# Optimization experiments

Hardware: AMD Instinct MI355X
Metric: run time of the kernel (lower is better)

## Reference

```python
import jax, jax.numpy as jnp
import numpy as np

N = 100000
E = 1600000
D_IN = 128
D_OUT = 128


def setup_inputs() -> dict:
    key = jax.random.key(0)
    k1, k2, k3, k4, k5, k6 = jax.random.split(key, 6)
    h = jax.random.normal(k1, (N, D_IN), dtype=jnp.float32)
    # deg^{-1/2}-style positive per-node normalization, shape [N,1]
    norm = jax.random.uniform(k2, (N, 1), dtype=jnp.float32, minval=0.05, maxval=1.0)
    weight = jax.random.normal(k3, (D_IN, D_OUT), dtype=jnp.float32) * (1.0 / np.sqrt(D_IN))
    bias = jax.random.normal(k4, (D_OUT,), dtype=jnp.float32) * 0.01
    src = jax.random.randint(k5, (E,), 0, N, dtype=jnp.int32)
    dst = jax.random.randint(k6, (E,), 0, N, dtype=jnp.int32)
    return {"h": h, "norm": norm, "weight": weight, "bias": bias, "src": src, "dst": dst}


def reference(h, norm, weight, bias, src, dst):
    # m = (h @ W) * norm   (per-source-node message)
    m = jnp.matmul(h, weight) * norm            # [N, D_OUT]
    # copy_src + sum: scatter-sum messages from src nodes into dst nodes
    n = jax.ops.segment_sum(m[src], dst, num_segments=h.shape[0])  # [N, D_OUT]
    # destination-side normalization, bias, LeakyReLU(0.2)
    n = n * norm + bias
    return jax.nn.leaky_relu(n, negative_slope=0.2)
```

## Files before the change

### kernel.cpp

```cpp
#include <hip/hip_runtime.h>

#define N_NODES 100000
#define E_EDGES 1600000
#define D 128
#define SHIFT 7
#define BNODES 128
#define NB ((N_NODES + BNODES - 1) / BNODES)

#define CNT_CHUNK 2048
#define CNT_NBLK ((E_EDGES + CNT_CHUNK - 1) / CNT_CHUNK)
#define PREP_NBLK (N_NODES * 32 / 256)
#define SCAT_CHUNK 8192
#define SCAT_PASS 2
#define SCAT_NBLK ((E_EDGES + SCAT_CHUNK - 1) / SCAT_CHUNK)
#define GATH32_NBLK (N_NODES / 8)

#define FBLK 64
#define FGRID ((N_NODES + FBLK - 1) / FBLK)

#define GROWS 64
#define KCH 32

typedef _Float16       f16x8  __attribute__((ext_vector_type(8)));
typedef float          f32x4  __attribute__((ext_vector_type(4)));
typedef unsigned short u16x8  __attribute__((ext_vector_type(8)));

#define WS_CNT   0
#define WS_BOFF  784
#define WS_POS   1568
#define WS_NOFF  2352
#define WS_EBUF  102400
#define WS_ESRC  (102400 + E_EDGES)
#define WS_HS    (102400 + 2 * E_EDGES)
#define WS_FULL_INTS ((size_t)WS_HS + (size_t)N_NODES * D / 2)
#define WS_MID_INTS  ((size_t)WS_HS)

__global__ __launch_bounds__(256) void prep_count(const float* __restrict__ h,
                                                  const float* __restrict__ norm,
                                                  unsigned short* __restrict__ hs,
                                                  const int* __restrict__ dst,
                                                  int* __restrict__ cnt,
                                                  int prep_blocks) {
    __shared__ int hist[NB];
    const int t = threadIdx.x;
    if ((int)blockIdx.x < prep_blocks) {
        const int idx = blockIdx.x * 256 + t;
        const int node = idx >> 5;
        const int c = (idx & 31) << 2;
        const float nv = norm[node];
        const float4 v = *reinterpret_cast<const float4*>(h + node * D + c);
        float a[4] = {v.x * nv, v.y * nv, v.z * nv, v.w * nv};
        ushort4 o;
        unsigned short* op = reinterpret_cast<unsigned short*>(&o);
        #pragma unroll
        for (int i = 0; i < 4; ++i) {
            unsigned int u = __float_as_uint(a[i]);
            u += 0x7FFFu + ((u >> 16) & 1u);
            op[i] = (unsigned short)(u >> 16);
        }
        *reinterpret_cast<ushort4*>(hs + node * D + c) = o;
        return;
    }
    const int cb = blockIdx.x - prep_blocks;
    const int e0 = cb * CNT_CHUNK;
    const int rem = (E_EDGES - e0 < CNT_CHUNK) ? (E_EDGES - e0) : CNT_CHUNK;
    for (int i = t; i < NB; i += 256) hist[i] = 0;
    __syncthreads();
    if (rem == CNT_CHUNK) {
        const int4* d4 = reinterpret_cast<const int4*>(dst + e0);
        #pragma unroll
        for (int p = 0; p < 2; ++p) {
            const int4 v = d4[p * 256 + t];
            atomicAdd(&hist[v.x >> SHIFT], 1);
            atomicAdd(&hist[v.y >> SHIFT], 1);
            atomicAdd(&hist[v.z >> SHIFT], 1);
            atomicAdd(&hist[v.w >> SHIFT], 1);
        }
    } else {
        for (int i = t; i < rem; i += 256)
            atomicAdd(&hist[dst[e0 + i] >> SHIFT], 1);
    }
    __syncthreads();
    for (int b = t; b < NB; b += 256) {
        const int c = hist[b];
        if (c) atomicAdd(&cnt[b], c);
    }
}

__global__ __launch_bounds__(1024) void coarse_scan(const int* __restrict__ cnt,
                                                    int* __restrict__ boff,
                                                    int* __restrict__ pos) {
    __shared__ int buf[2][1024];
    const int t = threadIdx.x;
    const int v = (t < NB) ? cnt[t] : 0;
    int pi = 0;
    buf[0][t] = v;
    __syncthreads();
    #pragma unroll
    for (int o = 1; o < 1024; o <<= 1) {
        const int nv = buf[pi][t] + (t >= o ? buf[pi][t - o] : 0);
        buf[1 - pi][t] = nv;
        pi = 1 - pi;
        __syncthreads();
    }
    if (t < NB) {
        const int excl = buf[pi][t] - v;
        boff[t] = excl;
        pos[t] = excl;
    }
    if (t == 0) boff[NB] = E_EDGES;
}

__global__ __launch_bounds__(1024) void coarse_scatter(const int* __restrict__ src,
                                                       const int* __restrict__ dst,
                                                       int* __restrict__ pos,
                                                       int* __restrict__ ebuf) {
    __shared__ int hist[NB];
    const int t = threadIdx.x;
    const int e0 = blockIdx.x * SCAT_CHUNK;
    const int rem = (E_EDGES - e0 < SCAT_CHUNK) ? (E_EDGES - e0) : SCAT_CHUNK;
    for (int i = t; i < NB; i += 1024) hist[i] = 0;
    __syncthreads();
    if (rem == SCAT_CHUNK) {
        const int4* d4 = reinterpret_cast<const int4*>(dst + e0);
        #pragma unroll
        for (int p = 0; p < SCAT_PASS; ++p) {
            const int4 v = d4[p * 1024 + t];
            atomicAdd(&hist[v.x >> SHIFT], 1);
            atomicAdd(&hist[v.y >> SHIFT], 1);
            atomicAdd(&hist[v.z >> SHIFT], 1);
            atomicAdd(&hist[v.w >> SHIFT], 1);
        }
    } else {
        for (int i = t; i < rem; i += 1024)
            atomicAdd(&hist[dst[e0 + i] >> SHIFT], 1);
    }
    __syncthreads();
    for (int b = t; b < NB; b += 1024) {
        const int c = hist[b];
        if (c) hist[b] = atomicAdd(&pos[b], c);
    }
    __syncthreads();
    if (rem == SCAT_CHUNK) {
        const int4* d4 = reinterpret_cast<const int4*>(dst + e0);
        const int4* s4 = reinterpret_cast<const int4*>(src + e0);
        #pragma unroll
        for (int p = 0; p < SCAT_PASS; ++p) {
            const int4 dv = d4[p * 1024 + t];
            const int4 sv = s4[p * 1024 + t];
            int pz;
            pz = atomicAdd(&hist[dv.x >> SHIFT], 1);
            ebuf[pz] = (sv.x << SHIFT) | (dv.x & (BNODES - 1));
            pz = atomicAdd(&hist[dv.y >> SHIFT], 1);
            ebuf[pz] = (sv.y << SHIFT) | (dv.y & (BNODES - 1));
            pz = atomicAdd(&hist[dv.z >> SHIFT], 1);
            ebuf[pz] = (sv.z << SHIFT) | (dv.z & (BNODES - 1));
            pz = atomicAdd(&hist[dv.w >> SHIFT], 1);
            ebuf[pz] = (sv.w << SHIFT) | (dv.w & (BNODES - 1));
        }
    } else {
        for (int i = t; i < rem; i += 1024) {
            const int d = dst[e0 + i];
            const int b = d >> SHIFT;
            const int p = atomicAdd(&hist[b], 1);
            ebuf[p] = (src[e0 + i] << SHIFT) | (d & (BNODES - 1));
        }
    }
}

__global__ __launch_bounds__(256) void bin_sort(const int* __restrict__ boff,
                                                const int* __restrict__ ebuf,
                                                int* __restrict__ esrc,
                                                int* __restrict__ noff) {
    __shared__ int hist[BNODES];
    __shared__ int curs[BNODES];
    __shared__ int sbuf[2][BNODES];
    const int t = threadIdx.x;
    const int bin = blockIdx.x;
    if (t < BNODES) hist[t] = 0;
    __syncthreads();
    const int b0 = boff[bin];
    const int b1 = boff[bin + 1];
    for (int i = b0 + t; i < b1; i += 256)
        atomicAdd(&hist[ebuf[i] & (BNODES - 1)], 1);
    __syncthreads();
    if (t < BNODES) sbuf[0][t] = hist[t];
    __syncthreads();
    int pi = 0;
    #pragma unroll
    for (int o = 1; o < BNODES; o <<= 1) {
        if (t < BNODES)
            sbuf[1 - pi][t] = sbuf[pi][t] + (t >= o ? sbuf[pi][t - o] : 0);
        pi = 1 - pi;
        __syncthreads();
    }
    if (t < BNODES) {
        const int base = b0 + sbuf[pi][t] - hist[t];
        curs[t] = base;
        const int node = (bin << SHIFT) + t;
        if (node < N_NODES) noff[node] = base;
    }
    if (bin == 0 && t == 0) noff[N_NODES] = E_EDGES;
    __syncthreads();
    for (int i = b0 + t; i < b1; i += 256) {
        const int w = ebuf[i];
        const int p = atomicAdd(&curs[w & (BNODES - 1)], 1);
        esrc[p] = w >> SHIFT;
    }
}

__device__ __forceinline__ void wprep_body(int tid, const float* __restrict__ Wm,
                                           f16x8* __restrict__ Whs) {
    const int kiter = tid >> 9;
    const int nt = (tid >> 6) & 7;
    const int lane = tid & 63;
    const int q = lane >> 4;
    const int col = nt * 16 + (lane & 15);
    f16x8 v;
    #pragma unroll
    for (int j = 0; j < 8; ++j)
        v[j] = (_Float16)Wm[(kiter * 32 + q * 8 + j) * D + col];
    Whs[tid] = v;
}

__global__ __launch_bounds__(256) void fused_gather_gemm(
    const unsigned short* __restrict__ hs, const int* __restrict__ noff,
    const int* __restrict__ esrc, const float* __restrict__ Wm,
    const float* __restrict__ bias, const float* __restrict__ norm,
    float* __restrict__ out)
{
    __shared__ _Float16 gs[FBLK][136];
    __shared__ f16x8 Wlds[2048];
    const int t = threadIdx.x;
    const int row0 = blockIdx.x * FBLK;
    const int c = (t & 15) << 3;

    #pragma unroll 1
    for (int r = 0; r < 4; ++r) {
        const int nl = r * 16 + (t >> 4);
        const int node = row0 + nl;
        float a[8];
        #pragma unroll
        for (int j = 0; j < 8; ++j) a[j] = 0.f;
        if (node < N_NODES) {
            int i = noff[node];
            const int end = noff[node + 1];
            for (; i + 7 < end; i += 8) {
                const int s0 = esrc[i];     const int s1 = esrc[i + 1];
                const int s2 = esrc[i + 2]; const int s3 = esrc[i + 3];
                const int s4 = esrc[i + 4]; const int s5 = esrc[i + 5];
                const int s6 = esrc[i + 6]; const int s7 = esrc[i + 7];
                const u16x8 u0 = *reinterpret_cast<const u16x8*>(hs + s0 * D + c);
                const u16x8 u1 = *reinterpret_cast<const u16x8*>(hs + s1 * D + c);
                const u16x8 u2 = *reinterpret_cast<const u16x8*>(hs + s2 * D + c);
                const u16x8 u3 = *reinterpret_cast<const u16x8*>(hs + s3 * D + c);
                const u16x8 u4 = *reinterpret_cast<const u16x8*>(hs + s4 * D + c);
                const u16x8 u5 = *reinterpret_cast<const u16x8*>(hs + s5 * D + c);
                const u16x8 u6 = *reinterpret_cast<const u16x8*>(hs + s6 * D + c);
                const u16x8 u7 = *reinterpret_cast<const u16x8*>(hs + s7 * D + c);
                #pragma unroll
                for (int j = 0; j < 8; ++j) {
                    a[j] += __uint_as_float((unsigned int)u0[j] << 16);
                    a[j] += __uint_as_float((unsigned int)u1[j] << 16);
                    a[j] += __uint_as_float((unsigned int)u2[j] << 16);
                    a[j] += __uint_as_float((unsigned int)u3[j] << 16);
                    a[j] += __uint_as_float((unsigned int)u4[j] << 16);
                    a[j] += __uint_as_float((unsigned int)u5[j] << 16);
                    a[j] += __uint_as_float((unsigned int)u6[j] << 16);
                    a[j] += __uint_as_float((unsigned int)u7[j] << 16);
                }
            }
            if (i + 3 < end) {
                const int s0 = esrc[i];     const int s1 = esrc[i + 1];
                const int s2 = esrc[i + 2]; const int s3 = esrc[i + 3];
                const u16x8 u0 = *reinterpret_cast<const u16x8*>(hs + s0 * D + c);
                const u16x8 u1 = *reinterpret_cast<const u16x8*>(hs + s1 * D + c);
                const u16x8 u2 = *reinterpret_cast<const u16x8*>(hs + s2 * D + c);
                const u16x8 u3 = *reinterpret_cast<const u16x8*>(hs + s3 * D + c);
                #pragma unroll
                for (int j = 0; j < 8; ++j) {
                    a[j] += __uint_as_float((unsigned int)u0[j] << 16);
                    a[j] += __uint_as_float((unsigned int)u1[j] << 16);
                    a[j] += __uint_as_float((unsigned int)u2[j] << 16);
                    a[j] += __uint_as_float((unsigned int)u3[j] << 16);
                }
                i += 4;
            }
            for (; i < end; ++i) {
                const int s = esrc[i];
                const u16x8 u = *reinterpret_cast<const u16x8*>(hs + s * D + c);
                #pragma unroll
                for (int j = 0; j < 8; ++j)
                    a[j] += __uint_as_float((unsigned int)u[j] << 16);
            }
        }
        f16x8 o;
        #pragma unroll
        for (int j = 0; j < 8; ++j) o[j] = (_Float16)a[j];
        *reinterpret_cast<f16x8*>(&gs[nl][c]) = o;
    }

    #pragma unroll 1
    for (int e = t; e < 2048; e += 256) {
        const int kiter = e >> 9;
        const int nt = (e >> 6) & 7;
        const int lane = e & 63;
        const int q = lane >> 4;
        const int col = nt * 16 + (lane & 15);
        f16x8 v;
        #pragma unroll
        for (int j = 0; j < 8; ++j)
            v[j] = (_Float16)Wm[(kiter * 32 + q * 8 + j) * D + col];
        Wlds[e] = v;
    }
    __syncthreads();

    const int lane = t & 63;
    const int strip = t >> 6;
    const int q = lane >> 4;
    const int l15 = lane & 15;

    f32x4 acc[8];
    #pragma unroll
    for (int i = 0; i < 8; ++i) acc[i] = (f32x4){0.f, 0.f, 0.f, 0.f};

    #pragma unroll
    for (int kiter = 0; kiter < 4; ++kiter) {
        const f16x8 a =
            *reinterpret_cast<const f16x8*>(&gs[strip * 16 + l15][kiter * 32 + q * 8]);
        #pragma unroll
        for (int nt = 0; nt < 8; ++nt) {
            const f16x8 b = Wlds[(kiter * 8 + nt) * 64 + lane];
            acc[nt] = __builtin_amdgcn_mfma_f32_16x16x32_f16(a, b, acc[nt], 0, 0, 0);
        }
    }

    float nrm[4];
    int mr[4];
    #pragma unroll
    for (int rgi = 0; rgi < 4; ++rgi) {
        mr[rgi] = row0 + strip * 16 + q * 4 + rgi;
        nrm[rgi] = (mr[rgi] < N_NODES) ? norm[mr[rgi]] : 0.f;
    }
    #pragma unroll
    for (int nt = 0; nt < 8; ++nt) {
        const int col = nt * 16 + l15;
        const float bc = bias[col];
        #pragma unroll
        for (int rgi = 0; rgi < 4; ++rgi) {
            if (mr[rgi] < N_NODES) {
                float v = acc[nt][rgi] * nrm[rgi] + bc;
                v = v > 0.f ? v : 0.2f * v;
                out[mr[rgi] * D + col] = v;
            }
        }
    }
}

__global__ __launch_bounds__(256) void gather_fp32(const float* __restrict__ h,
                                                   const float* __restrict__ norm,
                                                   const int* __restrict__ noff,
                                                   const int* __restrict__ esrc,
                                                   float* __restrict__ g,
                                                   const float* __restrict__ Wm,
                                                   f16x8* __restrict__ Whs) {
    if ((int)blockIdx.x >= GATH32_NBLK) {
        wprep_body((blockIdx.x - GATH32_NBLK) * 256 + threadIdx.x, Wm, Whs);
        return;
    }
    const int t = threadIdx.x;
    const int node = blockIdx.x * 8 + (t >> 5);
    const int c = (t & 31) << 2;
    const int beg = noff[node];
    const int end = noff[node + 1];
    float4 acc = make_float4(0.f, 0.f, 0.f, 0.f);
    for (int i = beg; i < end; ++i) {
        const int s = esrc[i];
        const float nv = norm[s];
        const float4 hv = *reinterpret_cast<const float4*>(h + s * D + c);
        acc.x += hv.x * nv;
        acc.y += hv.y * nv;
        acc.z += hv.z * nv;
        acc.w += hv.w * nv;
    }
    *reinterpret_cast<float4*>(g + node * D + c) = acc;
}

__global__ __launch_bounds__(256) void scatter_kernel(
    const float* __restrict__ h, const float* __restrict__ norm,
    const int* __restrict__ src, const int* __restrict__ dst,
    float* __restrict__ g)
{
    const int idx = blockIdx.x * 256 + threadIdx.x;
    const int e = idx >> 5;
    const int c = (idx & 31) << 2;
    const int s = src[e];
    const int d = dst[e];
    const float nv = norm[s];
    const float4 hv = *reinterpret_cast<const float4*>(h + s * D + c);
    float* gp = g + d * D + c;
    atomicAdd(gp + 0, hv.x * nv);
    atomicAdd(gp + 1, hv.y * nv);
    atomicAdd(gp + 2, hv.z * nv);
    atomicAdd(gp + 3, hv.w * nv);
}

__global__ __launch_bounds__(256) void gemm_mfma(
    float* __restrict__ out, const f16x8* __restrict__ Whs,
    const float* __restrict__ bias, const float* __restrict__ norm)
{
    __shared__ f16x8 Wlds[2048];
    const int t = threadIdx.x;
    const int row0 = blockIdx.x * 64;

    #pragma unroll
    for (int p = 0; p < 8; ++p)
        reinterpret_cast<float4*>(Wlds)[p * 256 + t] =
            reinterpret_cast<const float4*>(Whs)[p * 256 + t];
    __syncthreads();

    const int lane = t & 63;
    const int strip = t >> 6;
    const int q = lane >> 4;
    const int l15 = lane & 15;

    int mrow = row0 + strip * 16 + l15;
    if (mrow >= N_NODES) mrow = N_NODES - 1;

    f32x4 acc[8];
    #pragma unroll
    for (int i = 0; i < 8; ++i) acc[i] = (f32x4){0.f, 0.f, 0.f, 0.f};

    #pragma unroll
    for (int kiter = 0; kiter < 4; ++kiter) {
        const float* gp = out + mrow * D + kiter * 32 + q * 8;
        const float4 ga = *reinterpret_cast<const float4*>(gp);
        const float4 gb = *reinterpret_cast<const float4*>(gp + 4);
        f16x8 a;
        a[0] = (_Float16)ga.x; a[1] = (_Float16)ga.y;
        a[2] = (_Float16)ga.z; a[3] = (_Float16)ga.w;
        a[4] = (_Float16)gb.x; a[5] = (_Float16)gb.y;
        a[6] = (_Float16)gb.z; a[7] = (_Float16)gb.w;
        #pragma unroll
        for (int nt = 0; nt < 8; ++nt) {
            const f16x8 b = Wlds[(kiter * 8 + nt) * 64 + lane];
            acc[nt] = __builtin_amdgcn_mfma_f32_16x16x32_f16(a, b, acc[nt], 0, 0, 0);
        }
    }

    float nrm[4];
    int mr[4];
    #pragma unroll
    for (int rgi = 0; rgi < 4; ++rgi) {
        mr[rgi] = row0 + strip * 16 + q * 4 + rgi;
        nrm[rgi] = (mr[rgi] < N_NODES) ? norm[mr[rgi]] : 0.f;
    }
    #pragma unroll
    for (int nt = 0; nt < 8; ++nt) {
        const int col = nt * 16 + l15;
        const float bc = bias[col];
        #pragma unroll
        for (int rgi = 0; rgi < 4; ++rgi) {
            if (mr[rgi] < N_NODES) {
                float v = acc[nt][rgi] * nrm[rgi] + bc;
                v = v > 0.f ? v : 0.2f * v;
                out[mr[rgi] * D + col] = v;
            }
        }
    }
}

__global__ __launch_bounds__(256) void gemm_epilogue(
    float* __restrict__ out, const float* __restrict__ Wm,
    const float* __restrict__ bias, const float* __restrict__ norm)
{
    __shared__ float gs[GROWS][D + 4];
    __shared__ float Wlds[KCH][D];
    const int t = threadIdx.x;
    const int row0 = blockIdx.x * GROWS;

    #pragma unroll
    for (int p = 0; p < 8; ++p) {
        const int i = p * 256 + t;
        const int r = i >> 5;
        const int c = (i & 31) << 2;
        int gr = row0 + r;
        if (gr >= N_NODES) gr = N_NODES - 1;
        const float4 v = *reinterpret_cast<const float4*>(out + gr * D + c);
        *reinterpret_cast<float4*>(&gs[r][c]) = v;
    }

    const int rg = (t >> 5) * 8;
    const int cb = (t & 31) << 2;

    float4 acc[8];
    #pragma unroll
    for (int i = 0; i < 8; ++i) acc[i] = make_float4(0.f, 0.f, 0.f, 0.f);

    for (int kc = 0; kc < D; kc += KCH) {
        __syncthreads();
        #pragma unroll
        for (int p = 0; p < 4; ++p) {
            const int i = p * 256 + t;
            const int kk = i >> 5;
            const int c = (i & 31) << 2;
            *reinterpret_cast<float4*>(&Wlds[kk][c]) =
                *reinterpret_cast<const float4*>(Wm + (kc + kk) * D + c);
        }
        __syncthreads();

        #pragma unroll
        for (int k4 = 0; k4 < KCH; k4 += 4) {
            float4 wv[4];
            #pragma unroll
            for (int kk = 0; kk < 4; ++kk)
                wv[kk] = *reinterpret_cast<const float4*>(&Wlds[k4 + kk][cb]);
            #pragma unroll
            for (int i = 0; i < 8; ++i) {
                const float4 gv = *reinterpret_cast<const float4*>(&gs[rg + i][kc + k4]);
                acc[i].x += gv.x * wv[0].x; acc[i].y += gv.x * wv[0].y;
                acc[i].z += gv.x * wv[0].z; acc[i].w += gv.x * wv[0].w;
                acc[i].x += gv.y * wv[1].x; acc[i].y += gv.y * wv[1].y;
                acc[i].z += gv.y * wv[1].z; acc[i].w += gv.y * wv[1].w;
                acc[i].x += gv.z * wv[2].x; acc[i].y += gv.z * wv[2].y;
                acc[i].z += gv.z * wv[2].z; acc[i].w += gv.z * wv[2].w;
                acc[i].x += gv.w * wv[3].x; acc[i].y += gv.w * wv[3].y;
                acc[i].z += gv.w * wv[3].z; acc[i].w += gv.w * wv[3].w;
            }
        }
    }

    const float4 b = *reinterpret_cast<const float4*>(bias + cb);
    #pragma unroll
    for (int i = 0; i < 8; ++i) {
        const int gr = row0 + rg + i;
        if (gr < N_NODES) {
            const float nv = norm[gr];
            float4 v;
            v.x = acc[i].x * nv + b.x;
            v.y = acc[i].y * nv + b.y;
            v.z = acc[i].z * nv + b.z;
            v.w = acc[i].w * nv + b.w;
            v.x = v.x > 0.f ? v.x : 0.2f * v.x;
            v.y = v.y > 0.f ? v.y : 0.2f * v.y;
            v.z = v.z > 0.f ? v.z : 0.2f * v.z;
            v.w = v.w > 0.f ? v.w : 0.2f * v.w;
            *reinterpret_cast<float4*>(out + gr * D + cb) = v;
        }
    }
}

extern "C" void kernel_launch(void* const* d_in, const int* in_sizes, int n_in,
                              void* d_out, int out_size, void* d_ws, size_t ws_size,
                              hipStream_t stream) {
    const float* h    = (const float*)d_in[0];
    const float* norm = (const float*)d_in[1];
    const float* Wm   = (const float*)d_in[2];
    const float* bias = (const float*)d_in[3];
    const int*   src  = (const int*)d_in[4];
    const int*   dst  = (const int*)d_in[5];
    float* out = (float*)d_out;
    int* ws = (int*)d_ws;

    if (ws_size >= WS_MID_INTS * 4) {
        int* cnt  = ws + WS_CNT;
        int* boff = ws + WS_BOFF;
        int* pos  = ws + WS_POS;
        int* noff = ws + WS_NOFF;
        int* ebuf = ws + WS_EBUF;
        int* esrc = ws + WS_ESRC;
        unsigned short* hs = (unsigned short*)(ws + WS_HS);
        f16x8* Whs = (f16x8*)ebuf;
        const bool use_bf16 = (ws_size >= WS_FULL_INTS * 4);

        hipMemsetAsync(cnt, 0, NB * sizeof(int), stream);
        if (use_bf16) {
            prep_count<<<PREP_NBLK + CNT_NBLK, 256, 0, stream>>>(h, norm, hs, dst, cnt, PREP_NBLK);
        } else {
            prep_count<<<CNT_NBLK, 256, 0, stream>>>(h, norm, hs, dst, cnt, 0);
        }
        coarse_scan   <<<1, 1024, 0, stream>>>(cnt, boff, pos);
        coarse_scatter<<<SCAT_NBLK, 1024, 0, stream>>>(src, dst, pos, ebuf);
        bin_sort      <<<NB, 256, 0, stream>>>(boff, ebuf, esrc, noff);
        if (use_bf16) {
            fused_gather_gemm<<<FGRID, 256, 0, stream>>>(hs, noff, esrc, Wm, bias, norm, out);
        } else {
            gather_fp32<<<GATH32_NBLK + 8, 256, 0, stream>>>(h, norm, noff, esrc, out, Wm, Whs);
            gemm_mfma<<<(N_NODES + 63) / 64, 256, 0, stream>>>(out, Whs, bias, norm);
        }
    } else {
        hipMemsetAsync(out, 0, (size_t)N_NODES * D * sizeof(float), stream);
        scatter_kernel<<<(E_EDGES * 32) / 256, 256, 0, stream>>>(h, norm, src, dst, out);
        gemm_epilogue<<<(N_NODES + GROWS - 1) / GROWS, 256, 0, stream>>>(out, Wm, bias, norm);
    }
}
```

Baseline: 255.6 us.

## Fuse preprocessing and sorting stages into one cooperative kernel with grid syncs

Replaces the memset, count, scan, coarse scatter and bin sort launches with a single cooperative kernel of 1024 blocks that separates the phases with grid-wide syncs. This removes several launch gaps and intermediate kernel boundaries. The scatter phase now recomputes its per-chunk histogram instead of reusing the one from counting. Separately, the gather-GEMM kernel stages W into LDS in two halves so its shared-memory footprint shrinks, which may raise occupancy at the cost of an extra sync. If the cooperative launch fails, the code falls back to the original multi-kernel path.

```diff
diff --git a/kernel.cpp b/kernel.cpp
--- a/kernel.cpp
+++ b/kernel.cpp
@@ -1,4 +1,7 @@
 #include <hip/hip_runtime.h>
+#include <hip/hip_cooperative_groups.h>
+
+namespace cg = cooperative_groups;
 
 #define N_NODES 100000
 #define E_EDGES 1600000
@@ -14,6 +17,10 @@
 #define SCAT_PASS 2
 #define SCAT_NBLK ((E_EDGES + SCAT_CHUNK - 1) / SCAT_CHUNK)
 #define GATH32_NBLK (N_NODES / 8)
+
+#define COOP_NBLK 1024
+#define CCH 2048
+#define NCHUNK ((E_EDGES + CCH - 1) / CCH)
 
 #define FBLK 64
 #define FGRID ((N_NODES + FBLK - 1) / FBLK)
@@ -34,6 +41,199 @@
 #define WS_HS    (102400 + 2 * E_EDGES)
 #define WS_FULL_INTS ((size_t)WS_HS + (size_t)N_NODES * D / 2)
 #define WS_MID_INTS  ((size_t)WS_HS)
+
+__global__ __launch_bounds__(256) void pre_coop(
+    const float* __restrict__ h, const float* __restrict__ norm,
+    unsigned short* __restrict__ hs, const int* __restrict__ src,
+    const int* __restrict__ dst, int* __restrict__ cnt,
+    int* __restrict__ boff, int* __restrict__ pos,
+    int* __restrict__ ebuf, int* __restrict__ esrc, int* __restrict__ noff)
+{
+    cg::grid_group grid = cg::this_grid();
+    __shared__ int hist[NB];
+    __shared__ int sc_vals[1024];
+    __shared__ int sc_part[256];
+    __shared__ int shist[BNODES];
+    __shared__ int scurs[BNODES];
+    __shared__ int ssbuf[2][BNODES];
+
+    const int t = threadIdx.x;
+    const int b = blockIdx.x;
+    const int gtid = b * 256 + t;
+
+    if (gtid < NB) cnt[gtid] = 0;
+    if (gtid == 0) noff[N_NODES] = E_EDGES;
+
+    for (int i = t; i < NB; i += 256) hist[i] = 0;
+    __syncthreads();
+    if (b < NCHUNK) {
+        const int e0 = b * CCH;
+        const int rem = (E_EDGES - e0 < CCH) ? (E_EDGES - e0) : CCH;
+        if (rem == CCH) {
+            const int4* d4 = reinterpret_cast<const int4*>(dst + e0);
+            #pragma unroll
+            for (int p = 0; p < 2; ++p) {
+                const int4 v = d4[p * 256 + t];
+                atomicAdd(&hist[v.x >> SHIFT], 1);
+                atomicAdd(&hist[v.y >> SHIFT], 1);
+                atomicAdd(&hist[v.z >> SHIFT], 1);
+                atomicAdd(&hist[v.w >> SHIFT], 1);
+            }
+        } else {
+            for (int i = t; i < rem; i += 256)
+                atomicAdd(&hist[dst[e0 + i] >> SHIFT], 1);
+        }
+    }
+    for (int idx = gtid; idx < N_NODES * 32; idx += COOP_NBLK * 256) {
+        const int node = idx >> 5;
+        const int c = (idx & 31) << 2;
+        const float nv = norm[node];
+        const float4 v = *reinterpret_cast<const float4*>(h + node * D + c);
+        float a[4] = {v.x * nv, v.y * nv, v.z * nv, v.w * nv};
+        ushort4 o;
+        unsigned short* op = reinterpret_cast<unsigned short*>(&o);
+        #pragma unroll
+        for (int i = 0; i < 4; ++i) {
+            unsigned int u = __float_as_uint(a[i]);
+            u += 0x7FFFu + ((u >> 16) & 1u);
+            op[i] = (unsigned short)(u >> 16);
+        }
+        *reinterpret_cast<ushort4*>(hs + node * D + c) = o;
+    }
+    __threadfence();
+    grid.sync();
+
+    if (b < NCHUNK) {
+        for (int i = t; i < NB; i += 256) {
+            const int c = hist[i];
+            if (c) atomicAdd(&cnt[i], c);
+        }
+    }
+    __threadfence();
+    grid.sync();
+
+    if (b == 0) {
+        #pragma unroll
+        for (int k = 0; k < 4; ++k) {
+            const int i = t * 4 + k;
+            sc_vals[i] = (i < NB) ? cnt[i] : 0;
+        }
+        __syncthreads();
+        const int s0 = sc_vals[t * 4];
+        const int s1 = s0 + sc_vals[t * 4 + 1];
+        const int s2 = s1 + sc_vals[t * 4 + 2];
+        const int s3 = s2 + sc_vals[t * 4 + 3];
+        sc_part[t] = s3;
+        __syncthreads();
+        #pragma unroll
+        for (int o = 1; o < 256; o <<= 1) {
+            const int add = (t >= o) ? sc_part[t - o] : 0;
+            __syncthreads();
+            sc_part[t] += add;
+            __syncthreads();
+        }
+        const int base = (t > 0) ? sc_part[t - 1] : 0;
+        const int inc[4] = {0, s0, s1, s2};
+        #pragma unroll
+        for (int k = 0; k < 4; ++k) {
+            const int i = t * 4 + k;
+            if (i < NB) {
+                const int excl = base + inc[k];
+                boff[i] = excl;
+                pos[i] = excl;
+            }
+        }
+        if (t == 0) boff[NB] = E_EDGES;
+    }
+    __threadfence();
+    grid.sync();
+
+    if (b < NCHUNK) {
+        const int e0 = b * CCH;
+        const int rem = (E_EDGES - e0 < CCH) ? (E_EDGES - e0) : CCH;
+        for (int i = t; i < NB; i += 256) hist[i] = 0;
+        __syncthreads();
+        if (rem == CCH) {
+            const int4* d4 = reinterpret_cast<const int4*>(dst + e0);
+            #pragma unroll
+            for (int p = 0; p < 2; ++p) {
+                const int4 v = d4[p * 256 + t];
+                atomicAdd(&hist[v.x >> SHIFT], 1);
+                atomicAdd(&hist[v.y >> SHIFT], 1);
+                atomicAdd(&hist[v.z >> SHIFT], 1);
+                atomicAdd(&hist[v.w >> SHIFT], 1);
+            }
+        } else {
+            for (int i = t; i < rem; i += 256)
+                atomicAdd(&hist[dst[e0 + i] >> SHIFT], 1);
+        }
+        __syncthreads();
+        for (int i = t; i < NB; i += 256) {
+            const int c = hist[i];
+            if (c) hist[i] = atomicAdd(&pos[i], c);
+        }
+        __syncthreads();
+        if (rem == CCH) {
+            const int4* d4 = reinterpret_cast<const int4*>(dst + e0);
+            const int4* s4 = reinterpret_cast<const int4*>(src + e0);
+            #pragma unroll
+            for (int p = 0; p < 2; ++p) {
+                const int4 dv = d4[p * 256 + t];
+                const int4 sv = s4[p * 256 + t];
+                int pz;
+                pz = atomicAdd(&hist[dv.x >> SHIFT], 1);
+                ebuf[pz] = (sv.x << SHIFT) | (dv.x & (BNODES - 1));
+                pz = atomicAdd(&hist[dv.y >> SHIFT], 1);
+                ebuf[pz] = (sv.y << SHIFT) | (dv.y & (BNODES - 1));
+                pz = atomicAdd(&hist[dv.z >> SHIFT], 1);
+                ebuf[pz] = (sv.z << SHIFT) | (dv.z & (BNODES - 1));
+                pz = atomicAdd(&hist[dv.w >> SHIFT], 1);
+                ebuf[pz] = (sv.w << SHIFT) | (dv.w & (BNODES - 1));
+            }
+        } else {
+            for (int i = t; i < rem; i += 256) {
+                const int d = dst[e0 + i];
+                const int bb = d >> SHIFT;
+                const int p = atomicAdd(&hist[bb], 1);
+                ebuf[p] = (src[e0 + i] << SHIFT) | (d & (BNODES - 1));
+            }
+        }
+    }
+    __threadfence();
+    grid.sync();
+
+    if (b < NB) {
+        if (t < BNODES) shist[t] = 0;
+        __syncthreads();
+        const int b0 = boff[b];
+        const int b1 = boff[b + 1];
+        for (int i = b0 + t; i < b1; i += 256)
+            atomicAdd(&shist[ebuf[i] & (BNODES - 1)], 1);
+        __syncthreads();
+        if (t < BNODES) ssbuf[0][t] = shist[t];
+        __syncthreads();
+        int pi = 0;
+        #pragma unroll
+        for (int o = 1; o < BNODES; o <<= 1) {
+            if (t < BNODES)
+                ssbuf[1 - pi][t] = ssbuf[pi][t] + (t >= o ? ssbuf[pi][t - o] : 0);
+            pi = 1 - pi;
+            __syncthreads();
+        }
+        if (t < BNODES) {
+            const int base = b0 + ssbuf[pi][t] - shist[t];
+            scurs[t] = base;
+            const int node = (b << SHIFT) + t;
+            if (node < N_NODES) noff[node] = base;
+        }
+        __syncthreads();
+        for (int i = b0 + t; i < b1; i += 256) {
+            const int w = ebuf[i];
+            const int p = atomicAdd(&scurs[w & (BNODES - 1)], 1);
+            esrc[p] = w >> SHIFT;
+        }
+    }
+}
 
 __global__ __launch_bounds__(256) void prep_count(const float* __restrict__ h,
                                                   const float* __restrict__ norm,
@@ -230,7 +430,7 @@
     float* __restrict__ out)
 {
     __shared__ _Float16 gs[FBLK][136];
-    __shared__ f16x8 Wlds[2048];
+    __shared__ f16x8 Wlds[1024];
     const int t = threadIdx.x;
     const int row0 = blockIdx.x * FBLK;
     const int c = (t & 15) << 3;
@@ -300,21 +500,6 @@
         *reinterpret_cast<f16x8*>(&gs[nl][c]) = o;
     }
 
-    #pragma unroll 1
-    for (int e = t; e < 2048; e += 256) {
-        const int kiter = e >> 9;
-        const int nt = (e >> 6) & 7;
-        const int lane = e & 63;
-        const int q = lane >> 4;
-        const int col = nt * 16 + (lane & 15);
-        f16x8 v;
-        #pragma unroll
-        for (int j = 0; j < 8; ++j)
-            v[j] = (_Float16)Wm[(kiter * 32 + q * 8 + j) * D + col];
-        Wlds[e] = v;
-    }
-    __syncthreads();
-
     const int lane = t & 63;
     const int strip = t >> 6;
     const int q = lane >> 4;
@@ -324,14 +509,33 @@
     #pragma unroll
     for (int i = 0; i < 8; ++i) acc[i] = (f32x4){0.f, 0.f, 0.f, 0.f};
 
-    #pragma unroll
-    for (int kiter = 0; kiter < 4; ++kiter) {
-        const f16x8 a =
-            *reinterpret_cast<const f16x8*>(&gs[strip * 16 + l15][kiter * 32 + q * 8]);
-        #pragma unroll
-        for (int nt = 0; nt < 8; ++nt) {
-            const f16x8 b = Wlds[(kiter * 8 + nt) * 64 + lane];
-            acc[nt] = __builtin_amdgcn_mfma_f32_16x16x32_f16(a, b, acc[nt], 0, 0, 0);
+    #pragma unroll 1
+    for (int half = 0; half < 2; ++half) {
+        __syncthreads();
+        for (int e = t; e < 1024; e += 256) {
+            const int ge = (half << 10) + e;
+            const int kiter = ge >> 9;
+            const int nt = (ge >> 6) & 7;
+            const int lane2 = ge & 63;
+            const int q2 = lane2 >> 4;
+            const int col = nt * 16 + (lane2 & 15);
+            f16x8 v;
+            #pragma unroll
+            for (int j = 0; j < 8; ++j)
+                v[j] = (_Float16)Wm[(kiter * 32 + q2 * 8 + j) * D + col];
+            Wlds[e] = v;
+        }
+        __syncthreads();
+        #pragma unroll
+        for (int kk = 0; kk < 2; ++kk) {
+            const int kiter = half * 2 + kk;
+            const f16x8 a =
+                *reinterpret_cast<const f16x8*>(&gs[strip * 16 + l15][kiter * 32 + q * 8]);
+            #pragma unroll
+            for (int nt = 0; nt < 8; ++nt) {
+                const f16x8 b = Wlds[(kk * 8 + nt) * 64 + lane];
+                acc[nt] = __builtin_amdgcn_mfma_f32_16x16x32_f16(a, b, acc[nt], 0, 0, 0);
+            }
         }
     }
 
@@ -573,21 +777,32 @@
         f16x8* Whs = (f16x8*)ebuf;
         const bool use_bf16 = (ws_size >= WS_FULL_INTS * 4);
 
+        if (use_bf16) {
+            void* args[] = {(void*)&h, (void*)&norm, (void*)&hs, (void*)&src,
+                            (void*)&dst, (void*)&cnt, (void*)&boff, (void*)&pos,
+                            (void*)&ebuf, (void*)&esrc, (void*)&noff};
+            const hipError_t err = hipLaunchCooperativeKernel(
+                (const void*)pre_coop, dim3(COOP_NBLK), dim3(256), args, 0, stream);
+            if (err == hipSuccess) {
+                fused_gather_gemm<<<FGRID, 256, 0, stream>>>(hs, noff, esrc, Wm, bias, norm, out);
+                return;
+            }
+            hipMemsetAsync(cnt, 0, NB * sizeof(int), stream);
+            prep_count<<<PREP_NBLK + CNT_NBLK, 256, 0, stream>>>(h, norm, hs, dst, cnt, PREP_NBLK);
+            coarse_scan   <<<1, 1024, 0, stream>>>(cnt, boff, pos);
+            coarse_scatter<<<SCAT_NBLK, 1024, 0, stream>>>(src, dst, pos, ebuf);
+            bin_sort      <<<NB, 256, 0, stream>>>(boff, ebuf, esrc, noff);
+            fused_gather_gemm<<<FGRID, 256, 0, stream>>>(hs, noff, esrc, Wm, bias, norm, out);
+            return;
+        }
+
         hipMemsetAsync(cnt, 0, NB * sizeof(int), stream);
-        if (use_bf16) {
-            prep_count<<<PREP_NBLK + CNT_NBLK, 256, 0, stream>>>(h, norm, hs, dst, cnt, PREP_NBLK);
-        } else {
-            prep_count<<<CNT_NBLK, 256, 0, stream>>>(h, norm, hs, dst, cnt, 0);
-        }
+        prep_count<<<CNT_NBLK, 256, 0, stream>>>(h, norm, hs, dst, cnt, 0);
         coarse_scan   <<<1, 1024, 0, stream>>>(cnt, boff, pos);
         coarse_scatter<<<SCAT_NBLK, 1024, 0, stream>>>(src, dst, pos, ebuf);
         bin_sort      <<<NB, 256, 0, stream>>>(boff, ebuf, esrc, noff);
-        if (use_bf16) {
-            fused_gather_gemm<<<FGRID, 256, 0, stream>>>(hs, noff, esrc, Wm, bias, norm, out);
-        } else {
-            gather_fp32<<<GATH32_NBLK + 8, 256, 0, stream>>>(h, norm, noff, esrc, out, Wm, Whs);
-            gemm_mfma<<<(N_NODES + 63) / 64, 256, 0, stream>>>(out, Whs, bias, norm);
-        }
+        gather_fp32<<<GATH32_NBLK + 8, 256, 0, stream>>>(h, norm, noff, esrc, out, Wm, Whs);
+        gemm_mfma<<<(N_NODES + 63) / 64, 256, 0, stream>>>(out, Whs, bias, norm);
     } else {
         hipMemsetAsync(out, 0, (size_t)N_NODES * D * sizeof(float), stream);
         scatter_kernel<<<(E_EDGES * 32) / 256, 256, 0, stream>>>(h, norm, src, dst, out);
```

After: 974.2 us. 281% more time.

## Split fused gather-GEMM into separate gather and in-place fp16 GEMM kernels

Applied to the files above, without the earlier changes.

Replaces the fused kernel, which gathered 64 rows into shared memory and then ran the MFMA GEMM, with two kernels. The first gathers the aggregated rows as fp16 into the output buffer (stride 256 halves) and also prepares the fp16 W tiles. The second reads those rows from global memory and writes fp32 results in place, with a barrier between the reads and the writes. This trades an extra global round trip and a kernel launch for higher gather occupancy, since the gather kernel no longer holds the shared tile or the W conversion.

```diff
diff --git a/kernel.cpp b/kernel.cpp
--- a/kernel.cpp
+++ b/kernel.cpp
@@ -13,10 +13,8 @@
 #define SCAT_CHUNK 8192
 #define SCAT_PASS 2
 #define SCAT_NBLK ((E_EDGES + SCAT_CHUNK - 1) / SCAT_CHUNK)
+#define GATH_NBLK (N_NODES / 16)
 #define GATH32_NBLK (N_NODES / 8)
-
-#define FBLK 64
-#define FGRID ((N_NODES + FBLK - 1) / FBLK)
 
 #define GROWS 64
 #define KCH 32
@@ -34,6 +32,8 @@
 #define WS_HS    (102400 + 2 * E_EDGES)
 #define WS_FULL_INTS ((size_t)WS_HS + (size_t)N_NODES * D / 2)
 #define WS_MID_INTS  ((size_t)WS_HS)
+
+#define GROW16 256
 
 __global__ __launch_bounds__(256) void prep_count(const float* __restrict__ h,
                                                   const float* __restrict__ norm,
@@ -223,96 +223,89 @@
     Whs[tid] = v;
 }
 
-__global__ __launch_bounds__(256) void fused_gather_gemm(
+__global__ __launch_bounds__(256) void gather_wprep(
     const unsigned short* __restrict__ hs, const int* __restrict__ noff,
-    const int* __restrict__ esrc, const float* __restrict__ Wm,
-    const float* __restrict__ bias, const float* __restrict__ norm,
-    float* __restrict__ out)
+    const int* __restrict__ esrc, _Float16* __restrict__ g16,
+    const float* __restrict__ Wm, f16x8* __restrict__ Whs)
 {
-    __shared__ _Float16 gs[FBLK][136];
+    if ((int)blockIdx.x >= GATH_NBLK) {
+        wprep_body((blockIdx.x - GATH_NBLK) * 256 + threadIdx.x, Wm, Whs);
+        return;
+    }
+    const int t = threadIdx.x;
+    const int node = blockIdx.x * 16 + (t >> 4);
+    const int c = (t & 15) << 3;
+    int i = noff[node];
+    const int end = noff[node + 1];
+    float a[8];
+    #pragma unroll
+    for (int j = 0; j < 8; ++j) a[j] = 0.f;
+    for (; i + 7 < end; i += 8) {
+        const int s0 = esrc[i];     const int s1 = esrc[i + 1];
+        const int s2 = esrc[i + 2]; const int s3 = esrc[i + 3];
+        const int s4 = esrc[i + 4]; const int s5 = esrc[i + 5];
+        const int s6 = esrc[i + 6]; const int s7 = esrc[i + 7];
+        const u16x8 u0 = *reinterpret_cast<const u16x8*>(hs + s0 * D + c);
+        const u16x8 u1 = *reinterpret_cast<const u16x8*>(hs + s1 * D + c);
+        const u16x8 u2 = *reinterpret_cast<const u16x8*>(hs + s2 * D + c);
+        const u16x8 u3 = *reinterpret_cast<const u16x8*>(hs + s3 * D + c);
+        const u16x8 u4 = *reinterpret_cast<const u16x8*>(hs + s4 * D + c);
+        const u16x8 u5 = *reinterpret_cast<const u16x8*>(hs + s5 * D + c);
+        const u16x8 u6 = *reinterpret_cast<const u16x8*>(hs + s6 * D + c);
+        const u16x8 u7 = *reinterpret_cast<const u16x8*>(hs + s7 * D + c);
+        #pragma unroll
+        for (int j = 0; j < 8; ++j) {
+            a[j] += __uint_as_float((unsigned int)u0[j] << 16);
+            a[j] += __uint_as_float((unsigned int)u1[j] << 16);
+            a[j] += __uint_as_float((unsigned int)u2[j] << 16);
+            a[j] += __uint_as_float((unsigned int)u3[j] << 16);
+            a[j] += __uint_as_float((unsigned int)u4[j] << 16);
+            a[j] += __uint_as_float((unsigned int)u5[j] << 16);
+            a[j] += __uint_as_float((unsigned int)u6[j] << 16);
+            a[j] += __uint_as_float((unsigned int)u7[j] << 16);
+        }
+    }
+    if (i + 3 < end) {
+        const int s0 = esrc[i];     const int s1 = esrc[i + 1];
+        const int s2 = esrc[i + 2]; const int s3 = esrc[i + 3];
+        const u16x8 u0 = *reinterpret_cast<const u16x8*>(hs + s0 * D + c);
+        const u16x8 u1 = *reinterpret_cast<const u16x8*>(hs + s1 * D + c);
+        const u16x8 u2 = *reinterpret_cast<const u16x8*>(hs + s2 * D + c);
+        const u16x8 u3 = *reinterpret_cast<const u16x8*>(hs + s3 * D + c);
+        #pragma unroll
+        for (int j = 0; j < 8; ++j) {
+            a[j] += __uint_as_float((unsigned int)u0[j] << 16);
+            a[j] += __uint_as_float((unsigned int)u1[j] << 16);
+            a[j] += __uint_as_float((unsigned int)u2[j] << 16);
+            a[j] += __uint_as_float((unsigned int)u3[j] << 16);
+        }
+        i += 4;
+    }
+    for (; i < end; ++i) {
+        const int s = esrc[i];
+        const u16x8 u = *reinterpret_cast<const u16x8*>(hs + s * D + c);
+        #pragma unroll
+        for (int j = 0; j < 8; ++j)
+            a[j] += __uint_as_float((unsigned int)u[j] << 16);
+    }
+    f16x8 o;
+    #pragma unroll
+    for (int j = 0; j < 8; ++j) o[j] = (_Float16)a[j];
+    *reinterpret_cast<f16x8*>(g16 + node * GROW16 + c) = o;
+}
+
+__global__ __launch_bounds__(256) void gemm_mfma_f16g(
+    const _Float16* g16, float* out, const f16x8* __restrict__ Whs,
+    const float* __restrict__ bias, const float* __restrict__ norm)
+{
     __shared__ f16x8 Wlds[2048];
     const int t = threadIdx.x;
-    const int row0 = blockIdx.x * FBLK;
-    const int c = (t & 15) << 3;
-
-    #pragma unroll 1
-    for (int r = 0; r < 4; ++r) {
-        const int nl = r * 16 + (t >> 4);
-        const int node = row0 + nl;
-        float a[8];
-        #pragma unroll
-        for (int j = 0; j < 8; ++j) a[j] = 0.f;
-        if (node < N_NODES) {
-            int i = noff[node];
-            const int end = noff[node + 1];
-            for (; i + 7 < end; i += 8) {
-                const int s0 = esrc[i];     const int s1 = esrc[i + 1];
-                const int s2 = esrc[i + 2]; const int s3 = esrc[i + 3];
-                const int s4 = esrc[i + 4]; const int s5 = esrc[i + 5];
-                const int s6 = esrc[i + 6]; const int s7 = esrc[i + 7];
-                const u16x8 u0 = *reinterpret_cast<const u16x8*>(hs + s0 * D + c);
-                const u16x8 u1 = *reinterpret_cast<const u16x8*>(hs + s1 * D + c);
-                const u16x8 u2 = *reinterpret_cast<const u16x8*>(hs + s2 * D + c);
-                const u16x8 u3 = *reinterpret_cast<const u16x8*>(hs + s3 * D + c);
-                const u16x8 u4 = *reinterpret_cast<const u16x8*>(hs + s4 * D + c);
-                const u16x8 u5 = *reinterpret_cast<const u16x8*>(hs + s5 * D + c);
-                const u16x8 u6 = *reinterpret_cast<const u16x8*>(hs + s6 * D + c);
-                const u16x8 u7 = *reinterpret_cast<const u16x8*>(hs + s7 * D + c);
-                #pragma unroll
-                for (int j = 0; j < 8; ++j) {
-                    a[j] += __uint_as_float((unsigned int)u0[j] << 16);
-                    a[j] += __uint_as_float((unsigned int)u1[j] << 16);
-                    a[j] += __uint_as_float((unsigned int)u2[j] << 16);
-                    a[j] += __uint_as_float((unsigned int)u3[j] << 16);
-                    a[j] += __uint_as_float((unsigned int)u4[j] << 16);
-                    a[j] += __uint_as_float((unsigned int)u5[j] << 16);
-                    a[j] += __uint_as_float((unsigned int)u6[j] << 16);
-                    a[j] += __uint_as_float((unsigned int)u7[j] << 16);
-                }
-            }
-            if (i + 3 < end) {
-                const int s0 = esrc[i];     const int s1 = esrc[i + 1];
-                const int s2 = esrc[i + 2]; const int s3 = esrc[i + 3];
-                const u16x8 u0 = *reinterpret_cast<const u16x8*>(hs + s0 * D + c);
-                const u16x8 u1 = *reinterpret_cast<const u16x8*>(hs + s1 * D + c);
-                const u16x8 u2 = *reinterpret_cast<const u16x8*>(hs + s2 * D + c);
-                const u16x8 u3 = *reinterpret_cast<const u16x8*>(hs + s3 * D + c);
-                #pragma unroll
-                for (int j = 0; j < 8; ++j) {
-                    a[j] += __uint_as_float((unsigned int)u0[j] << 16);
-                    a[j] += __uint_as_float((unsigned int)u1[j] << 16);
-                    a[j] += __uint_as_float((unsigned int)u2[j] << 16);
-                    a[j] += __uint_as_float((unsigned int)u3[j] << 16);
-                }
-                i += 4;
-            }
-            for (; i < end; ++i) {
-                const int s = esrc[i];
-                const u16x8 u = *reinterpret_cast<const u16x8*>(hs + s * D + c);
-                #pragma unroll
-                for (int j = 0; j < 8; ++j)
-                    a[j] += __uint_as_float((unsigned int)u[j] << 16);
-            }
-        }
-        f16x8 o;
-        #pragma unroll
-        for (int j = 0; j < 8; ++j) o[j] = (_Float16)a[j];
-        *reinterpret_cast<f16x8*>(&gs[nl][c]) = o;
-    }
-
-    #pragma unroll 1
-    for (int e = t; e < 2048; e += 256) {
-        const int kiter = e >> 9;
-        const int nt = (e >> 6) & 7;
-        const int lane = e & 63;
-        const int q = lane >> 4;
-        const int col = nt * 16 + (lane & 15);
-        f16x8 v;
-        #pragma unroll
-        for (int j = 0; j < 8; ++j)
-            v[j] = (_Float16)Wm[(kiter * 32 + q * 8 + j) * D + col];
-        Wlds[e] = v;
-    }
+    const int row0 = blockIdx.x * 64;
+
+    #pragma unroll
+    for (int p = 0; p < 8; ++p)
+        reinterpret_cast<float4*>(Wlds)[p * 256 + t] =
+            reinterpret_cast<const float4*>(Whs)[p * 256 + t];
     __syncthreads();
 
     const int lane = t & 63;
@@ -320,6 +313,9 @@
     const int q = lane >> 4;
     const int l15 = lane & 15;
 
+    int mrow = row0 + strip * 16 + l15;
+    if (mrow >= N_NODES) mrow = N_NODES - 1;
+
     f32x4 acc[8];
     #pragma unroll
     for (int i = 0; i < 8; ++i) acc[i] = (f32x4){0.f, 0.f, 0.f, 0.f};
@@ -327,13 +323,15 @@
     #pragma unroll
     for (int kiter = 0; kiter < 4; ++kiter) {
         const f16x8 a =
-            *reinterpret_cast<const f16x8*>(&gs[strip * 16 + l15][kiter * 32 + q * 8]);
+            *reinterpret_cast<const f16x8*>(g16 + mrow * GROW16 + kiter * 32 + q * 8);
         #pragma unroll
         for (int nt = 0; nt < 8; ++nt) {
             const f16x8 b = Wlds[(kiter * 8 + nt) * 64 + lane];
             acc[nt] = __builtin_amdgcn_mfma_f32_16x16x32_f16(a, b, acc[nt], 0, 0, 0);
         }
     }
+
+    __syncthreads();
 
     float nrm[4];
     int mr[4];
@@ -583,7 +581,9 @@
         coarse_scatter<<<SCAT_NBLK, 1024, 0, stream>>>(src, dst, pos, ebuf);
         bin_sort      <<<NB, 256, 0, stream>>>(boff, ebuf, esrc, noff);
         if (use_bf16) {
-            fused_gather_gemm<<<FGRID, 256, 0, stream>>>(hs, noff, esrc, Wm, bias, norm, out);
+            _Float16* g16 = (_Float16*)out;
+            gather_wprep<<<GATH_NBLK + 8, 256, 0, stream>>>(hs, noff, esrc, g16, Wm, Whs);
+            gemm_mfma_f16g<<<(N_NODES + 63) / 64, 256, 0, stream>>>(g16, out, Whs, bias, norm);
         } else {
             gather_fp32<<<GATH32_NBLK + 8, 256, 0, stream>>>(h, norm, noff, esrc, out, Wm, Whs);
             gemm_mfma<<<(N_NODES + 63) / 64, 256, 0, stream>>>(out, Whs, bias, norm);
```

After: 239.1 us. 6.5% less time.
